# Kernel tuning notes

Hardware: AMD Instinct MI355X
Metric: run time of the kernel (lower is better)

Reference implementation:

```python
import jax, jax.numpy as jnp
import numpy as np

NUM_EXPERTS = 64


def setup_inputs() -> dict:
    key = jax.random.key(0)
    k1, k2 = jax.random.split(key)
    x = jax.random.normal(k1, (8192, 4096), dtype=jnp.float32)
    W = jax.random.normal(k2, (NUM_EXPERTS, 4096), dtype=jnp.float32) * 0.02
    return {"x": x, "W": W}


def reference(x, W):
    # gate: logits = x @ W^T  -> [T, E]
    logits = jnp.einsum('th,eh->te', x, W)
    scores = jax.nn.softmax(logits, axis=-1)
    # top_k == 1 path: max with keepdim (torch scores.max(dim=-1, keepdim=True))
    expert_weights = jnp.max(scores, axis=-1, keepdims=True)      # [T, 1]
    expert_indices = jnp.argmax(scores, axis=-1, keepdims=True)   # [T, 1] int
    # routing_counts = bincount(expert_indices.squeeze(1), minlength=E)
    routing_counts = jnp.bincount(expert_indices[:, 0], length=NUM_EXPERTS)
    return (expert_weights, expert_indices, scores, routing_counts)
```

## Files before the change

kernel.cpp:

```cpp
#include <hip/hip_runtime.h>
#include <stdint.h>

#define T_TOKENS 8192
#define K_DIM    4096
#define NEXP     64
#define TB       128

typedef short bf16x8 __attribute__((ext_vector_type(8)));
typedef float f32x4  __attribute__((ext_vector_type(4)));

__device__ __forceinline__ uint32_t f2bf(float v) {
    uint32_t u = __builtin_bit_cast(uint32_t, v);
    return (u + 0x7fffu + ((u >> 16) & 1u)) >> 16;
}
__device__ __forceinline__ float bf2f(uint32_t b) {
    return __builtin_bit_cast(float, b << 16);
}
struct S3 { short h, l, q; };
__device__ __forceinline__ S3 cvt1(float v) {
    uint32_t hb = f2bf(v); float r  = v - bf2f(hb);
    uint32_t lb = f2bf(r); float r2 = r - bf2f(lb);
    uint32_t qb = f2bf(r2);
    S3 o; o.h = (short)hb; o.l = (short)lb; o.q = (short)qb; return o;
}
__device__ __forceinline__ void cvt8(const float4 a0, const float4 a1,
                                     bf16x8& xh, bf16x8& xl, bf16x8& xq) {
    const float av[8] = {a0.x, a0.y, a0.z, a0.w, a1.x, a1.y, a1.z, a1.w};
#pragma unroll
    for (int j = 0; j < 8; ++j) {
        S3 o = cvt1(av[j]);
        xh[j] = o.h; xl[j] = o.l; xq[j] = o.q;
    }
}

__global__ void wpack(const float* __restrict__ W, float4* __restrict__ Wf,
                      float* __restrict__ out_counts) {
    const int l     = threadIdx.x;
    const int kstep = blockIdx.x;
    const int etile = blockIdx.y;
    if (kstep == 0 && etile == 0)
        out_counts[l] = 0.f;
    const int e = etile * 16 + (l & 15);
    const int k = kstep * 32 + (l >> 4) * 8;
    const float* src = W + (size_t)e * K_DIM + k;
    bf16x8 h, l1, l2;
#pragma unroll
    for (int j = 0; j < 8; ++j) {
        S3 o = cvt1(src[j]);
        h[j] = o.h; l1[j] = o.l; l2[j] = o.q;
    }
    const size_t base = ((size_t)(kstep * 4 + etile) * 3) * 64 + l;
    Wf[base]       = __builtin_bit_cast(float4, h);
    Wf[base + 64]  = __builtin_bit_cast(float4, l1);
    Wf[base + 128] = __builtin_bit_cast(float4, l2);
}

template <int NCH>
__global__ __launch_bounds__(512, 2) void gemm_mfma(
    const float*  __restrict__ x,
    const float4* __restrict__ Wf,
    float* __restrict__ P)
{
    const int tid  = threadIdx.x;
    const int l    = tid & 63;
    const int wv   = __builtin_amdgcn_readfirstlane(tid >> 6);
    const int rg   = wv >> 1;
    const int cg   = wv & 1;
    const int slice = blockIdx.x;
    const int t0    = blockIdx.y * TB;
    const int k0    = slice * (NCH * 32);

    const float4* x4 = (const float4*)x;
    const size_t xr0 = (size_t)(t0 + rg * 32 + (l & 15)) * (K_DIM / 4)
                     + (size_t)(k0 >> 2) + ((l >> 4) * 2);
    const size_t xr1 = xr0 + (size_t)16 * (K_DIM / 4);
    const float4* bb = Wf + (((size_t)(k0 >> 5) * 4 + cg * 2) * 3) * 64 + l;

    f32x4 acc00 = {0,0,0,0}, acc01 = {0,0,0,0};
    f32x4 acc10 = {0,0,0,0}, acc11 = {0,0,0,0};

    float4 xs[3][4];
    float4 bs[3][6];

#define LOADK(ks, slot)                                                        \
    do {                                                                       \
        const size_t xo = (size_t)(ks) * 8;                                    \
        xs[slot][0] = x4[xr0 + xo];     xs[slot][1] = x4[xr0 + xo + 1];        \
        xs[slot][2] = x4[xr1 + xo];     xs[slot][3] = x4[xr1 + xo + 1];        \
        const float4* bp = bb + (size_t)(ks) * 768;                            \
        bs[slot][0] = bp[0];   bs[slot][1] = bp[64];  bs[slot][2] = bp[128];   \
        bs[slot][3] = bp[192]; bs[slot][4] = bp[256]; bs[slot][5] = bp[320];   \
    } while (0)

    LOADK(0, 0);
    LOADK(1, 1);

#pragma unroll
    for (int ks = 0; ks < NCH; ++ks) {
        if (ks + 2 < NCH) LOADK(ks + 2, (ks + 2) % 3);
        const int s = ks % 3;

        bf16x8 xh0, xl0, xq0, xh1, xl1, xq1;
        cvt8(xs[s][0], xs[s][1], xh0, xl0, xq0);
        cvt8(xs[s][2], xs[s][3], xh1, xl1, xq1);

#pragma unroll
        for (int e = 0; e < 2; ++e) {
            bf16x8 wh = __builtin_bit_cast(bf16x8, bs[s][e * 3 + 0]);
            bf16x8 wl = __builtin_bit_cast(bf16x8, bs[s][e * 3 + 1]);
            bf16x8 wq = __builtin_bit_cast(bf16x8, bs[s][e * 3 + 2]);
            f32x4& a0 = e ? acc10 : acc00;
            f32x4& a1 = e ? acc11 : acc01;
            a0 = __builtin_amdgcn_mfma_f32_16x16x32_bf16(xh0, wh, a0, 0, 0, 0);
            a0 = __builtin_amdgcn_mfma_f32_16x16x32_bf16(xh0, wl, a0, 0, 0, 0);
            a0 = __builtin_amdgcn_mfma_f32_16x16x32_bf16(xh0, wq, a0, 0, 0, 0);
            a0 = __builtin_amdgcn_mfma_f32_16x16x32_bf16(xl0, wh, a0, 0, 0, 0);
            a0 = __builtin_amdgcn_mfma_f32_16x16x32_bf16(xl0, wl, a0, 0, 0, 0);
            a0 = __builtin_amdgcn_mfma_f32_16x16x32_bf16(xq0, wh, a0, 0, 0, 0);
            a1 = __builtin_amdgcn_mfma_f32_16x16x32_bf16(xh1, wh, a1, 0, 0, 0);
            a1 = __builtin_amdgcn_mfma_f32_16x16x32_bf16(xh1, wl, a1, 0, 0, 0);
            a1 = __builtin_amdgcn_mfma_f32_16x16x32_bf16(xh1, wq, a1, 0, 0, 0);
            a1 = __builtin_amdgcn_mfma_f32_16x16x32_bf16(xl1, wh, a1, 0, 0, 0);
            a1 = __builtin_amdgcn_mfma_f32_16x16x32_bf16(xl1, wl, a1, 0, 0, 0);
            a1 = __builtin_amdgcn_mfma_f32_16x16x32_bf16(xq1, wh, a1, 0, 0, 0);
        }
    }
#undef LOADK

    float* Pp = P + (size_t)slice * T_TOKENS * NEXP;
#pragma unroll
    for (int e = 0; e < 2; ++e) {
#pragma unroll
        for (int rt = 0; rt < 2; ++rt) {
            const f32x4 a = e ? (rt ? acc11 : acc10) : (rt ? acc01 : acc00);
            const int ecol = (cg * 2 + e) * 16 + (l & 15);
#pragma unroll
            for (int i = 0; i < 4; ++i) {
                int t = t0 + rg * 32 + rt * 16 + (l >> 4) * 4 + i;
                Pp[(size_t)t * NEXP + ecol] = a[i];
            }
        }
    }
}

template <int S>
__global__ __launch_bounds__(256) void router_finish_t(
    const float* __restrict__ P, float* __restrict__ out)
{
    const int lane = threadIdx.x & 63;
    const int wv   = threadIdx.x >> 6;
    const int t    = blockIdx.x * 4 + wv;

    float lg = 0.f;
#pragma unroll
    for (int s = 0; s < S; ++s)
        lg += P[((size_t)s * T_TOKENS + t) * NEXP + lane];

    float* out_w = out;
    float* out_i = out + T_TOKENS;
    float* out_s = out + 2 * T_TOKENS;
    float* out_c = out + 2 * T_TOKENS + (size_t)T_TOKENS * NEXP;

    float m = lg;
#pragma unroll
    for (int off = 32; off > 0; off >>= 1)
        m = fmaxf(m, __shfl_xor(m, off));
    float p = expf(lg - m);
    float s = p;
#pragma unroll
    for (int off = 32; off > 0; off >>= 1)
        s += __shfl_xor(s, off);
    float sc = p / s;

    float bv = sc; int bi = lane;
#pragma unroll
    for (int off = 32; off > 0; off >>= 1) {
        float ov = __shfl_xor(bv, off);
        int   oi = __shfl_xor(bi, off);
        if (ov > bv || (ov == bv && oi < bi)) { bv = ov; bi = oi; }
    }
    out_s[(size_t)t * NEXP + lane] = sc;
    if (lane == 0) {
        out_w[t] = bv;
        out_i[t] = (float)bi;
        atomicAdd(&out_c[bi], 1.0f);
    }
}

extern "C" void kernel_launch(void* const* d_in, const int* in_sizes, int n_in,
                              void* d_out, int out_size, void* d_ws, size_t ws_size,
                              hipStream_t stream)
{
    const float* x = (const float*)d_in[0];
    const float* W = (const float*)d_in[1];
    float* out = (float*)d_out;
    float* out_s = out + 2 * T_TOKENS;
    float* out_c = out + 2 * T_TOKENS + (size_t)T_TOKENS * NEXP;

    const size_t wf_bytes  = (size_t)128 * 4 * 3 * 64 * 16;
    const size_t per_slice = (size_t)T_TOKENS * NEXP * sizeof(float);

    int S = 8;
    while (S > 1 && wf_bytes + (size_t)S * per_slice > ws_size) S >>= 1;
    float4* Wf = (float4*)d_ws;
    float* Pbuf;
    if (wf_bytes + per_slice <= ws_size) {
        Pbuf = (float*)((char*)d_ws + wf_bytes);
    } else {
        S = 1;
        Pbuf = out_s;
    }

    wpack<<<dim3(128, 4), 64, 0, stream>>>(W, Wf, out_c);
    switch (S) {
        case 8: gemm_mfma<16> <<<dim3(8, T_TOKENS / TB), 512, 0, stream>>>(x, Wf, Pbuf); break;
        case 4: gemm_mfma<32> <<<dim3(4, T_TOKENS / TB), 512, 0, stream>>>(x, Wf, Pbuf); break;
        case 2: gemm_mfma<64> <<<dim3(2, T_TOKENS / TB), 512, 0, stream>>>(x, Wf, Pbuf); break;
        default: gemm_mfma<128><<<dim3(1, T_TOKENS / TB), 512, 0, stream>>>(x, Wf, Pbuf); break;
    }
    switch (S) {
        case 8: router_finish_t<8><<<T_TOKENS / 4, 256, 0, stream>>>(Pbuf, out); break;
        case 4: router_finish_t<4><<<T_TOKENS / 4, 256, 0, stream>>>(Pbuf, out); break;
        case 2: router_finish_t<2><<<T_TOKENS / 4, 256, 0, stream>>>(Pbuf, out); break;
        default: router_finish_t<1><<<T_TOKENS / 4, 256, 0, stream>>>(Pbuf, out); break;
    }
}
```

Baseline: 110.4 us.

## Stage x and W tiles through LDS with async global_load_lds ring buffer

Rewrites the split-K GEMM to copy x and packed W chunks straight into a 4-deep shared-memory ring using global_load_lds, with hand-placed vmcnt waits and barriers. x rows are XOR-swizzled to avoid bank conflicts. Each wave now owns 16 token rows and all 64 experts, so each x element is converted to bf16 triples once instead of twice. The aim is coalesced loads, less register pressure and latency hidden by a deeper prefetch. The cost is two barriers per chunk, 112 KB of LDS that drops occupancy to one block per CU, and fragile hard-coded waitcnt counts.

Measured after the change: 109.7 us. No clear change (-0.6%).

```diff
diff --git a/kernel.cpp b/kernel.cpp
--- a/kernel.cpp
+++ b/kernel.cpp
@@ -32,6 +32,11 @@
         xh[j] = o.h; xl[j] = o.l; xq[j] = o.q;
     }
 }
+
+#define GLDS(srcp, dstp) \
+    __builtin_amdgcn_global_load_lds( \
+        (const __attribute__((address_space(1))) void*)(srcp), \
+        (__attribute__((address_space(3))) void*)(dstp), 16, 0, 0)
 
 __global__ void wpack(const float* __restrict__ W, float4* __restrict__ Wf,
                       float* __restrict__ out_counts) {
@@ -56,89 +61,100 @@
 }
 
 template <int NCH>
-__global__ __launch_bounds__(512, 2) void gemm_mfma(
+__global__ __launch_bounds__(512, 1) void gemm_mfma(
     const float*  __restrict__ x,
     const float4* __restrict__ Wf,
     float* __restrict__ P)
 {
+    static_assert(NCH >= 4, "ring needs >=4 chunks");
+    __shared__ float4 xb[4][1024];
+    __shared__ float4 bb[4][768];
+
     const int tid  = threadIdx.x;
     const int l    = tid & 63;
     const int wv   = __builtin_amdgcn_readfirstlane(tid >> 6);
-    const int rg   = wv >> 1;
-    const int cg   = wv & 1;
     const int slice = blockIdx.x;
     const int t0    = blockIdx.y * TB;
     const int k0    = slice * (NCH * 32);
 
     const float4* x4 = (const float4*)x;
-    const size_t xr0 = (size_t)(t0 + rg * 32 + (l & 15)) * (K_DIM / 4)
-                     + (size_t)(k0 >> 2) + ((l >> 4) * 2);
-    const size_t xr1 = xr0 + (size_t)16 * (K_DIM / 4);
-    const float4* bb = Wf + (((size_t)(k0 >> 5) * 4 + cg * 2) * 3) * 64 + l;
-
-    f32x4 acc00 = {0,0,0,0}, acc01 = {0,0,0,0};
-    f32x4 acc10 = {0,0,0,0}, acc11 = {0,0,0,0};
-
-    float4 xs[3][4];
-    float4 bs[3][6];
-
-#define LOADK(ks, slot)                                                        \
-    do {                                                                       \
-        const size_t xo = (size_t)(ks) * 8;                                    \
-        xs[slot][0] = x4[xr0 + xo];     xs[slot][1] = x4[xr0 + xo + 1];        \
-        xs[slot][2] = x4[xr1 + xo];     xs[slot][3] = x4[xr1 + xo + 1];        \
-        const float4* bp = bb + (size_t)(ks) * 768;                            \
-        bs[slot][0] = bp[0];   bs[slot][1] = bp[64];  bs[slot][2] = bp[128];   \
-        bs[slot][3] = bp[192]; bs[slot][4] = bp[256]; bs[slot][5] = bp[320];   \
+    const int xrow = tid >> 3;
+    const int xcol = (tid & 7) ^ (xrow & 7);
+    const size_t xs0 = (size_t)(t0 + xrow) * (K_DIM / 4) + (size_t)(k0 >> 2) + xcol;
+    const size_t xs1 = xs0 + (size_t)64 * (K_DIM / 4);
+    const int kb0 = k0 >> 5;
+
+    const int r   = wv * 16 + (l & 15);
+    const int s0  = (l >> 4) * 2;
+    const int rx7 = r & 7;
+    const int ia0 = r * 8 + ((s0)     ^ rx7);
+    const int ia1 = r * 8 + ((s0 + 1) ^ rx7);
+
+    f32x4 acc[4];
+#pragma unroll
+    for (int et = 0; et < 4; ++et) acc[et] = (f32x4){0.f, 0.f, 0.f, 0.f};
+
+#define STAGE(c)                                                                \
+    do {                                                                        \
+        const int rg = (c) & 3;                                                 \
+        const size_t xo = (size_t)(c) * 8;                                      \
+        GLDS(x4 + xs0 + xo, &xb[rg][0 * 512 + wv * 64]);                        \
+        GLDS(x4 + xs1 + xo, &xb[rg][1 * 512 + wv * 64]);                        \
+        const size_t bo = (size_t)(kb0 + (c)) * 768;                            \
+        GLDS(Wf + bo + wv * 64 + l, &bb[rg][wv * 64]);                          \
+        if (wv < 4)                                                             \
+            GLDS(Wf + bo + 512 + wv * 64 + l, &bb[rg][512 + wv * 64]);          \
     } while (0)
 
-    LOADK(0, 0);
-    LOADK(1, 1);
-
-#pragma unroll
-    for (int ks = 0; ks < NCH; ++ks) {
-        if (ks + 2 < NCH) LOADK(ks + 2, (ks + 2) % 3);
-        const int s = ks % 3;
-
-        bf16x8 xh0, xl0, xq0, xh1, xl1, xq1;
-        cvt8(xs[s][0], xs[s][1], xh0, xl0, xq0);
-        cvt8(xs[s][2], xs[s][3], xh1, xl1, xq1);
-
-#pragma unroll
-        for (int e = 0; e < 2; ++e) {
-            bf16x8 wh = __builtin_bit_cast(bf16x8, bs[s][e * 3 + 0]);
-            bf16x8 wl = __builtin_bit_cast(bf16x8, bs[s][e * 3 + 1]);
-            bf16x8 wq = __builtin_bit_cast(bf16x8, bs[s][e * 3 + 2]);
-            f32x4& a0 = e ? acc10 : acc00;
-            f32x4& a1 = e ? acc11 : acc01;
-            a0 = __builtin_amdgcn_mfma_f32_16x16x32_bf16(xh0, wh, a0, 0, 0, 0);
-            a0 = __builtin_amdgcn_mfma_f32_16x16x32_bf16(xh0, wl, a0, 0, 0, 0);
-            a0 = __builtin_amdgcn_mfma_f32_16x16x32_bf16(xh0, wq, a0, 0, 0, 0);
-            a0 = __builtin_amdgcn_mfma_f32_16x16x32_bf16(xl0, wh, a0, 0, 0, 0);
-            a0 = __builtin_amdgcn_mfma_f32_16x16x32_bf16(xl0, wl, a0, 0, 0, 0);
-            a0 = __builtin_amdgcn_mfma_f32_16x16x32_bf16(xq0, wh, a0, 0, 0, 0);
-            a1 = __builtin_amdgcn_mfma_f32_16x16x32_bf16(xh1, wh, a1, 0, 0, 0);
-            a1 = __builtin_amdgcn_mfma_f32_16x16x32_bf16(xh1, wl, a1, 0, 0, 0);
-            a1 = __builtin_amdgcn_mfma_f32_16x16x32_bf16(xh1, wq, a1, 0, 0, 0);
-            a1 = __builtin_amdgcn_mfma_f32_16x16x32_bf16(xl1, wh, a1, 0, 0, 0);
-            a1 = __builtin_amdgcn_mfma_f32_16x16x32_bf16(xl1, wl, a1, 0, 0, 0);
-            a1 = __builtin_amdgcn_mfma_f32_16x16x32_bf16(xq1, wh, a1, 0, 0, 0);
+    STAGE(0); STAGE(1); STAGE(2);
+
+    for (int c = 0; c < NCH; ++c) {
+        __builtin_amdgcn_s_barrier();
+        if (c + 3 < NCH) STAGE(c + 3);
+
+        const int nb = (NCH - 1 - c < 3) ? (NCH - 1 - c) : 3;
+        if (wv < 4) {
+            if      (nb == 3) asm volatile("s_waitcnt vmcnt(12)" ::: "memory");
+            else if (nb == 2) asm volatile("s_waitcnt vmcnt(8)"  ::: "memory");
+            else if (nb == 1) asm volatile("s_waitcnt vmcnt(4)"  ::: "memory");
+            else              asm volatile("s_waitcnt vmcnt(0)"  ::: "memory");
+        } else {
+            if      (nb == 3) asm volatile("s_waitcnt vmcnt(9)"  ::: "memory");
+            else if (nb == 2) asm volatile("s_waitcnt vmcnt(6)"  ::: "memory");
+            else if (nb == 1) asm volatile("s_waitcnt vmcnt(3)"  ::: "memory");
+            else              asm volatile("s_waitcnt vmcnt(0)"  ::: "memory");
         }
-    }
-#undef LOADK
+        __builtin_amdgcn_s_barrier();
+
+        const int rg = c & 3;
+        float4 a0 = xb[rg][ia0];
+        float4 a1 = xb[rg][ia1];
+        bf16x8 xh, xl, xq;
+        cvt8(a0, a1, xh, xl, xq);
+
+#pragma unroll
+        for (int et = 0; et < 4; ++et) {
+            const float4* bp = &bb[rg][et * 192 + l];
+            bf16x8 wh = __builtin_bit_cast(bf16x8, bp[0]);
+            bf16x8 wl = __builtin_bit_cast(bf16x8, bp[64]);
+            bf16x8 wq = __builtin_bit_cast(bf16x8, bp[128]);
+            acc[et] = __builtin_amdgcn_mfma_f32_16x16x32_bf16(xh, wh, acc[et], 0, 0, 0);
+            acc[et] = __builtin_amdgcn_mfma_f32_16x16x32_bf16(xh, wl, acc[et], 0, 0, 0);
+            acc[et] = __builtin_amdgcn_mfma_f32_16x16x32_bf16(xh, wq, acc[et], 0, 0, 0);
+            acc[et] = __builtin_amdgcn_mfma_f32_16x16x32_bf16(xl, wh, acc[et], 0, 0, 0);
+            acc[et] = __builtin_amdgcn_mfma_f32_16x16x32_bf16(xl, wl, acc[et], 0, 0, 0);
+            acc[et] = __builtin_amdgcn_mfma_f32_16x16x32_bf16(xq, wh, acc[et], 0, 0, 0);
+        }
+    }
+#undef STAGE
 
     float* Pp = P + (size_t)slice * T_TOKENS * NEXP;
 #pragma unroll
-    for (int e = 0; e < 2; ++e) {
-#pragma unroll
-        for (int rt = 0; rt < 2; ++rt) {
-            const f32x4 a = e ? (rt ? acc11 : acc10) : (rt ? acc01 : acc00);
-            const int ecol = (cg * 2 + e) * 16 + (l & 15);
-#pragma unroll
-            for (int i = 0; i < 4; ++i) {
-                int t = t0 + rg * 32 + rt * 16 + (l >> 4) * 4 + i;
-                Pp[(size_t)t * NEXP + ecol] = a[i];
-            }
+    for (int et = 0; et < 4; ++et) {
+#pragma unroll
+        for (int i = 0; i < 4; ++i) {
+            int t = t0 + wv * 16 + (l >> 4) * 4 + i;
+            Pp[(size_t)t * NEXP + et * 16 + (l & 15)] = acc[et][i];
         }
     }
 }
```
